# Kernel optimization log

Hardware: AMD Instinct MI355X
Metric: run time of the kernel (lower is better)

Reference implementation:

```python
import math
import jax, jax.numpy as jnp
import numpy as np

B, S, D, L = 8, 4096, 1024, 16

def setup_inputs() -> dict:
    key = jax.random.key(0)
    k1, k2, k3 = jax.random.split(key, 3)
    memory = jax.random.normal(k1, (B, S, D), dtype=jnp.float32)
    summarizer = jax.random.normal(k2, (L, D), dtype=jnp.float32) * 0.02
    w_proj = jax.random.normal(k3, (1, L), dtype=jnp.float32) * (1.0 / math.sqrt(L))
    return {"memory": memory, "summarizer": summarizer, "w_proj": w_proj}

def reference(memory, summarizer, w_proj):
    # scores: [B, L, S] = summarizer @ memory^T / sqrt(D)
    d = summarizer.shape[-1]
    scores = jnp.einsum('ld,bsd->bls', summarizer, memory) / jnp.sqrt(jnp.asarray(d, memory.dtype))
    p_attn = jax.nn.softmax(scores, axis=-1)            # softmax over sequence S
    ctx = jnp.einsum('bls,bsd->bld', p_attn, memory)    # [B, L, D]
    # nn.Linear(L, 1, bias=False) applied to ctx.transpose(-1,-2): [B, D, L] @ W^T -> [B, D, 1]
    out = jnp.einsum('bld,l->bd', ctx, w_proj[0])       # [B, D]
    return out[:, None, :]                              # [B, 1, D] after final transpose
```

## Files before the change

kernel.cpp:

```cpp
#include <hip/hip_runtime.h>

#define SS 4096
#define DD 1024
#define LL 16
#define ROWF 1028

typedef __attribute__((ext_vector_type(8))) short short8;
typedef __attribute__((ext_vector_type(4))) float fl4;

static __device__ __forceinline__ short f2bf(float f) {
    unsigned u = __float_as_uint(f);
    u += 0x7FFFu + ((u >> 16) & 1u);
    return (short)(u >> 16);
}

static __device__ __forceinline__ short8 pack8(fl4 a, fl4 b) {
    short8 r;
    r[0] = f2bf(a[0]); r[1] = f2bf(a[1]); r[2] = f2bf(a[2]); r[3] = f2bf(a[3]);
    r[4] = f2bf(b[0]); r[5] = f2bf(b[1]); r[6] = f2bf(b[2]); r[7] = f2bf(b[3]);
    return r;
}

static __device__ __forceinline__ void dma16(const float* g, float* l) {
    __builtin_amdgcn_global_load_lds(
        (const __attribute__((address_space(1))) void*)g,
        (__attribute__((address_space(3))) void*)l, 16, 0, 0);
}

__global__ __launch_bounds__(512) void k_main(const float* __restrict__ mem,
                                              const float* __restrict__ summ,
                                              float* __restrict__ part,
                                              float* __restrict__ Zpart) {
    __shared__ float buf[4][8 * ROWF];
    __shared__ float e_lds[8 * LL];
    __shared__ float scr[8][256];

    int blk = blockIdx.x;
    int b   = blk >> 5;
    int s_base = (blk & 31) << 7;
    int t    = threadIdx.x;
    int wv   = t >> 6;
    int lane = t & 63;
    int o  = lane & 15;
    int qd = lane >> 4;

    const float* gseg = mem + ((size_t)b * SS + s_base) * DD;

    fl4 a0[4], a1[4];
    {
        const float* arow = summ + o * DD + wv * 128 + qd * 8;
        #pragma unroll
        for (int j = 0; j < 4; ++j) {
            a0[j] = *(const fl4*)(arow + j * 32);
            a1[j] = *(const fl4*)(arow + j * 32 + 4);
        }
    }
    short8 afr[4];
    #pragma unroll
    for (int j = 0; j < 4; ++j) afr[j] = pack8(a0[j], a1[j]);

    #pragma unroll
    for (int g0 = 0; g0 < 3; ++g0) {
        const float* gp = gseg + (size_t)g0 * 8 * DD;
        #pragma unroll
        for (int c = 0; c < 4; ++c)
            dma16(gp + (size_t)wv * DD + c * 256 + lane * 4,
                  &buf[g0][wv * ROWF + c * 256]);
    }

    int lg = t >> 8;
    int q  = t & 255;
    int s_sm = t & 7;
    int l_sm = (t >> 3) & 15;
    int scr_idx = ((l_sm >> 2) * 16 + s_sm) * 4 + (l_sm & 3);

    fl4 ctx[8];
    #pragma unroll
    for (int l = 0; l < 8; ++l) ctx[l] = (fl4){0.f, 0.f, 0.f, 0.f};
    float z = 0.f;
    const float scale = 0.03125f;

    for (int g = 0; g < 16; ++g) {
        if (g > 0) {
            const float* mrow = &buf[(g - 1) & 3][0] + q * 4;
            const fl4* erow = (const fl4*)&e_lds[lg * 8];
            #pragma unroll
            for (int s = 0; s < 8; ++s) {
                fl4 m4 = *(const fl4*)(mrow + s * ROWF);
                fl4 e0 = erow[s * 4];
                fl4 e1 = erow[s * 4 + 1];
                #pragma unroll
                for (int j = 0; j < 4; ++j) {
                    ctx[j]     += e0[j] * m4;
                    ctx[4 + j] += e1[j] * m4;
                }
            }
        }
        asm volatile("s_waitcnt lgkmcnt(0)" ::: "memory");
        if (g <= 13)      asm volatile("s_waitcnt vmcnt(8)" ::: "memory");
        else if (g == 14) asm volatile("s_waitcnt vmcnt(4)" ::: "memory");
        else              asm volatile("s_waitcnt vmcnt(0)" ::: "memory");
        __builtin_amdgcn_sched_barrier(0);
        __builtin_amdgcn_s_barrier();
        __builtin_amdgcn_sched_barrier(0);

        if (g <= 12) {
            const float* gp = gseg + (size_t)(g + 3) * 8 * DD;
            dma16(gp + (size_t)wv * DD +   0 + lane * 4, &buf[(g + 3) & 3][wv * ROWF +   0]);
            dma16(gp + (size_t)wv * DD + 256 + lane * 4, &buf[(g + 3) & 3][wv * ROWF + 256]);
            dma16(gp + (size_t)wv * DD + 512 + lane * 4, &buf[(g + 3) & 3][wv * ROWF + 512]);
            dma16(gp + (size_t)wv * DD + 768 + lane * 4, &buf[(g + 3) & 3][wv * ROWF + 768]);
        }
        __builtin_amdgcn_sched_barrier(0);

        const float* bbase = &buf[g & 3][0];
        fl4 acc = {0.f, 0.f, 0.f, 0.f};
        const float* brow = bbase + (o & 7) * ROWF + wv * 128 + qd * 8;
        #pragma unroll
        for (int j = 0; j < 4; ++j) {
            fl4 f0 = *(const fl4*)(brow + j * 32);
            fl4 f1 = *(const fl4*)(brow + j * 32 + 4);
            acc = __builtin_amdgcn_mfma_f32_16x16x32_bf16(afr[j], pack8(f0, f1),
                                                          acc, 0, 0, 0);
        }
        *(fl4*)&scr[wv][lane * 4] = acc;
        asm volatile("s_waitcnt lgkmcnt(0)" ::: "memory");
        __builtin_amdgcn_s_barrier();
        __builtin_amdgcn_sched_barrier(0);

        if (t < 128) {
            float sum = 0.f;
            #pragma unroll
            for (int w8 = 0; w8 < 8; ++w8) sum += scr[w8][scr_idx];
            float ev = __expf(sum * scale);
            e_lds[s_sm * LL + l_sm] = ev;
            z += ev;
        }
        asm volatile("s_waitcnt lgkmcnt(0)" ::: "memory");
        __builtin_amdgcn_s_barrier();
        __builtin_amdgcn_sched_barrier(0);
    }

    {
        const float* mrow = &buf[15 & 3][0] + q * 4;
        const fl4* erow = (const fl4*)&e_lds[lg * 8];
        #pragma unroll
        for (int s = 0; s < 8; ++s) {
            fl4 m4 = *(const fl4*)(mrow + s * ROWF);
            fl4 e0 = erow[s * 4];
            fl4 e1 = erow[s * 4 + 1];
            #pragma unroll
            for (int j = 0; j < 4; ++j) {
                ctx[j]     += e0[j] * m4;
                ctx[4 + j] += e1[j] * m4;
            }
        }
    }

    float* pp = part + (size_t)blk * LL * DD + (size_t)(lg * 8) * DD + q * 4;
    #pragma unroll
    for (int l = 0; l < 8; ++l) *(fl4*)(pp + (size_t)l * DD) = ctx[l];

    if (t < 128) {
        float v = z;
        v += __shfl_xor(v, 1, 64);
        v += __shfl_xor(v, 2, 64);
        v += __shfl_xor(v, 4, 64);
        if (s_sm == 0) Zpart[blk * LL + l_sm] = v;
    }
}

__global__ __launch_bounds__(256) void k_out(const float* __restrict__ part,
                                             const float* __restrict__ Zpart,
                                             const float* __restrict__ w,
                                             float* __restrict__ out) {
    int blkid = blockIdx.x;
    int b  = blkid >> 5;
    int d0 = (blkid & 31) << 5;
    int t = threadIdx.x;
    __shared__ float coef[LL];
    __shared__ fl4 red[32][8];

    if (t < LL) {
        float Z = 0.f;
        #pragma unroll
        for (int s = 0; s < 32; ++s) Z += Zpart[(b * 32 + s) * LL + t];
        coef[t] = w[t] / Z;
    }
    __syncthreads();

    int dq  = t & 7;
    int seg = t >> 3;
    const float* pb = part + (size_t)(b * 32 + seg) * LL * DD + d0 + dq * 4;
    fl4 acc = {0.f, 0.f, 0.f, 0.f};
    #pragma unroll
    for (int l = 0; l < LL; ++l) {
        fl4 v = *(const fl4*)(pb + (size_t)l * DD);
        float c = coef[l];
        acc += c * v;
    }
    red[seg][dq] = acc;
    __syncthreads();

    if (t < 8) {
        fl4 s = {0.f, 0.f, 0.f, 0.f};
        #pragma unroll
        for (int g = 0; g < 32; ++g) s += red[g][t];
        *(fl4*)&out[b * DD + d0 + t * 4] = s;
    }
}

extern "C" void kernel_launch(void* const* d_in, const int* in_sizes, int n_in,
                              void* d_out, int out_size, void* d_ws, size_t ws_size,
                              hipStream_t stream) {
    const float* mem  = (const float*)d_in[0];
    const float* summ = (const float*)d_in[1];
    const float* w    = (const float*)d_in[2];
    float* out = (float*)d_out;

    char* ws = (char*)d_ws;
    float* Zpart = (float*)ws;
    float* part  = (float*)(ws + 64 * 1024);

    k_main<<<256, 512, 0, stream>>>(mem, summ, part, Zpart);
    k_out<<<256, 256, 0, stream>>>(part, Zpart, w, out);
}
```

Measured before the change: 209.9 us.

## Split sequence across twice as many blocks with double-buffered LDS pipeline

Launches 512 blocks of 64 sequence rows each instead of 256 blocks of 128, and cuts the LDS ring from four buffers to two, so more blocks can be resident per CU. The aim is better CU coverage and occupancy while streaming the 128 MB memory tensor. In exchange the prefetch depth drops to one stage with an extra barrier per step, and the partial-context buffer and second-stage reduction double in size.

```diff
diff --git a/kernel.cpp b/kernel.cpp
--- a/kernel.cpp
+++ b/kernel.cpp
@@ -27,17 +27,17 @@
         (__attribute__((address_space(3))) void*)l, 16, 0, 0);
 }
 
-__global__ __launch_bounds__(512) void k_main(const float* __restrict__ mem,
-                                              const float* __restrict__ summ,
-                                              float* __restrict__ part,
-                                              float* __restrict__ Zpart) {
-    __shared__ float buf[4][8 * ROWF];
+__global__ __launch_bounds__(512, 4) void k_main(const float* __restrict__ mem,
+                                                 const float* __restrict__ summ,
+                                                 float* __restrict__ part,
+                                                 float* __restrict__ Zpart) {
+    __shared__ float buf[2][8 * ROWF];
     __shared__ float e_lds[8 * LL];
     __shared__ float scr[8][256];
 
     int blk = blockIdx.x;
-    int b   = blk >> 5;
-    int s_base = (blk & 31) << 7;
+    int b   = blk >> 6;
+    int s_base = (blk & 63) << 6;
     int t    = threadIdx.x;
     int wv   = t >> 6;
     int lane = t & 63;
@@ -60,13 +60,9 @@
     for (int j = 0; j < 4; ++j) afr[j] = pack8(a0[j], a1[j]);
 
     #pragma unroll
-    for (int g0 = 0; g0 < 3; ++g0) {
-        const float* gp = gseg + (size_t)g0 * 8 * DD;
-        #pragma unroll
-        for (int c = 0; c < 4; ++c)
-            dma16(gp + (size_t)wv * DD + c * 256 + lane * 4,
-                  &buf[g0][wv * ROWF + c * 256]);
-    }
+    for (int c = 0; c < 4; ++c)
+        dma16(gseg + (size_t)wv * DD + c * 256 + lane * 4,
+              &buf[0][wv * ROWF + c * 256]);
 
     int lg = t >> 8;
     int q  = t & 255;
@@ -80,9 +76,9 @@
     float z = 0.f;
     const float scale = 0.03125f;
 
-    for (int g = 0; g < 16; ++g) {
+    for (int g = 0; g < 8; ++g) {
         if (g > 0) {
-            const float* mrow = &buf[(g - 1) & 3][0] + q * 4;
+            const float* mrow = &buf[(g - 1) & 1][0] + q * 4;
             const fl4* erow = (const fl4*)&e_lds[lg * 8];
             #pragma unroll
             for (int s = 0; s < 8; ++s) {
@@ -97,23 +93,26 @@
             }
         }
         asm volatile("s_waitcnt lgkmcnt(0)" ::: "memory");
-        if (g <= 13)      asm volatile("s_waitcnt vmcnt(8)" ::: "memory");
-        else if (g == 14) asm volatile("s_waitcnt vmcnt(4)" ::: "memory");
-        else              asm volatile("s_waitcnt vmcnt(0)" ::: "memory");
-        __builtin_amdgcn_sched_barrier(0);
-        __builtin_amdgcn_s_barrier();
-        __builtin_amdgcn_sched_barrier(0);
-
-        if (g <= 12) {
-            const float* gp = gseg + (size_t)(g + 3) * 8 * DD;
-            dma16(gp + (size_t)wv * DD +   0 + lane * 4, &buf[(g + 3) & 3][wv * ROWF +   0]);
-            dma16(gp + (size_t)wv * DD + 256 + lane * 4, &buf[(g + 3) & 3][wv * ROWF + 256]);
-            dma16(gp + (size_t)wv * DD + 512 + lane * 4, &buf[(g + 3) & 3][wv * ROWF + 512]);
-            dma16(gp + (size_t)wv * DD + 768 + lane * 4, &buf[(g + 3) & 3][wv * ROWF + 768]);
-        }
-        __builtin_amdgcn_sched_barrier(0);
-
-        const float* bbase = &buf[g & 3][0];
+        __builtin_amdgcn_sched_barrier(0);
+        __builtin_amdgcn_s_barrier();
+        __builtin_amdgcn_sched_barrier(0);
+
+        if (g < 7) {
+            const float* gp = gseg + (size_t)(g + 1) * 8 * DD;
+            float* nb = &buf[(g + 1) & 1][wv * ROWF];
+            dma16(gp + (size_t)wv * DD +   0 + lane * 4, nb +   0);
+            dma16(gp + (size_t)wv * DD + 256 + lane * 4, nb + 256);
+            dma16(gp + (size_t)wv * DD + 512 + lane * 4, nb + 512);
+            dma16(gp + (size_t)wv * DD + 768 + lane * 4, nb + 768);
+            asm volatile("s_waitcnt vmcnt(4)" ::: "memory");
+        } else {
+            asm volatile("s_waitcnt vmcnt(0)" ::: "memory");
+        }
+        __builtin_amdgcn_sched_barrier(0);
+        __builtin_amdgcn_s_barrier();
+        __builtin_amdgcn_sched_barrier(0);
+
+        const float* bbase = &buf[g & 1][0];
         fl4 acc = {0.f, 0.f, 0.f, 0.f};
         const float* brow = bbase + (o & 7) * ROWF + wv * 128 + qd * 8;
         #pragma unroll
@@ -142,7 +141,7 @@
     }
 
     {
-        const float* mrow = &buf[15 & 3][0] + q * 4;
+        const float* mrow = &buf[7 & 1][0] + q * 4;
         const fl4* erow = (const fl4*)&e_lds[lg * 8];
         #pragma unroll
         for (int s = 0; s < 8; ++s) {
@@ -184,22 +183,24 @@
     if (t < LL) {
         float Z = 0.f;
         #pragma unroll
-        for (int s = 0; s < 32; ++s) Z += Zpart[(b * 32 + s) * LL + t];
+        for (int s = 0; s < 64; ++s) Z += Zpart[(b * 64 + s) * LL + t];
         coef[t] = w[t] / Z;
     }
     __syncthreads();
 
-    int dq  = t & 7;
-    int seg = t >> 3;
-    const float* pb = part + (size_t)(b * 32 + seg) * LL * DD + d0 + dq * 4;
+    int dq = t & 7;
+    int sg = t >> 3;
     fl4 acc = {0.f, 0.f, 0.f, 0.f};
     #pragma unroll
-    for (int l = 0; l < LL; ++l) {
-        fl4 v = *(const fl4*)(pb + (size_t)l * DD);
-        float c = coef[l];
-        acc += c * v;
-    }
-    red[seg][dq] = acc;
+    for (int h = 0; h < 2; ++h) {
+        const float* pb = part + (size_t)(b * 64 + sg + h * 32) * LL * DD + d0 + dq * 4;
+        #pragma unroll
+        for (int l = 0; l < LL; ++l) {
+            fl4 v = *(const fl4*)(pb + (size_t)l * DD);
+            acc += coef[l] * v;
+        }
+    }
+    red[sg][dq] = acc;
     __syncthreads();
 
     if (t < 8) {
@@ -222,6 +223,6 @@
     float* Zpart = (float*)ws;
     float* part  = (float*)(ws + 64 * 1024);
 
-    k_main<<<256, 512, 0, stream>>>(mem, summ, part, Zpart);
+    k_main<<<512, 512, 0, stream>>>(mem, summ, part, Zpart);
     k_out<<<256, 256, 0, stream>>>(part, Zpart, w, out);
 }
```

Measured after the change: 282.4 us. 1.35x slower.
